# Kernel tuning notes

Hardware: AMD Instinct MI355X
Metric: run time of the kernel (lower is better)

The kernel has to match this reference:

```python
import jax, jax.numpy as jnp
import numpy as np

N = 100_000       # nodes
E = 1_600_000     # edges (avg degree 16)
D = 64            # in_dim
H = 64            # hidden width (hidden_channels = [64,64,64,64] -> 3 GCN layers)
L = 3             # num GCNConv layers
END = 128         # end_channels
EPS = 1e-5        # batchnorm eps


def setup_inputs() -> dict:
    key = jax.random.key(0)
    ks = jax.random.split(key, 8)

    def lin(k, fi, fo):
        return (jax.random.normal(k, (fi, fo), jnp.float32) / np.sqrt(fi)).astype(jnp.float32)

    X = jax.random.normal(ks[0], (N, D), jnp.float32)
    edge_index = jax.random.randint(ks[1], (2, E), 0, N)
    W_in = lin(ks[2], D, H)
    b_in = jnp.zeros((H,), jnp.float32)
    Ws = (jax.random.normal(ks[3], (L, H, H), jnp.float32) / np.sqrt(H)).astype(jnp.float32)
    bs = jnp.zeros((L, H), jnp.float32)
    gammas = jnp.ones((L, H), jnp.float32)
    betas = jnp.zeros((L, H), jnp.float32)
    W1 = lin(ks[4], H, END)
    b1 = jnp.zeros((END,), jnp.float32)
    W2 = lin(ks[5], END, 1)
    b2 = jnp.zeros((1,), jnp.float32)
    return dict(X=X, edge_index=edge_index, W_in=W_in, b_in=b_in, Ws=Ws, bs=bs,
                gammas=gammas, betas=betas, W1=W1, b1=b1, W2=W2, b2=b2)


def reference(X, edge_index, W_in, b_in, Ws, bs, gammas, betas, W1, b1, W2, b2):
    src, dst = edge_index[0], edge_index[1]
    # symmetric GCN normalization with self-loops: deg includes the self-loop (+1)
    deg = jax.ops.segment_sum(jnp.ones((E,), X.dtype), dst, num_segments=N) + 1.0
    dinv = jax.lax.rsqrt(deg)                      # deg^{-1/2}
    norm = dinv[src] * dinv[dst]                   # [E]
    self_norm = (dinv * dinv)[:, None]             # deg^{-1} for self-loop edges, [N,1]

    x = X @ W_in + b_in                            # input Linear
    for i in range(L):
        h = x @ Ws[i]                              # [N, H]
        # gather -> weight -> scatter-add (neighbor aggregation) + self-loop term + bias
        agg = jax.ops.segment_sum(h[src] * norm[:, None], dst, num_segments=N)
        h = agg + h * self_norm + bs[i]
        # BatchNorm over nodes (training-mode batch statistics)
        mean = jnp.mean(h, axis=0)
        var = jnp.var(h, axis=0)
        h = gammas[i] * (h - mean) * jax.lax.rsqrt(var + EPS) + betas[i]
        if i < L - 1:
            h = jax.nn.relu(h)
        x = h
    # OutputLayer: Linear -> act -> Linear(n_steps=1), binary=False -> no sigmoid
    h = jax.nn.relu(x @ W1 + b1)
    return h @ W2 + b2
```

## Files before the change

kernel.cpp:

```cpp
#include <hip/hip_runtime.h>

#define NN 100000
#define NE 1600000
#define NB_SCAN 391

typedef __attribute__((ext_vector_type(8))) short bf16x8;
typedef __attribute__((ext_vector_type(4))) float f32x4;

__device__ inline float b2f(unsigned short u) {
  return __uint_as_float(((unsigned)u) << 16);
}
__device__ inline unsigned short f2b(float f) {
  unsigned x = __float_as_uint(f);
  unsigned r = (x + 0x7fffu + ((x >> 16) & 1u)) >> 16;
  return (unsigned short)r;
}


__global__ void count_rank_kernel(const int* __restrict__ dst, int* __restrict__ counts,
                                  int* __restrict__ rank) {
  int i = blockIdx.x * blockDim.x + threadIdx.x;
  int st = gridDim.x * blockDim.x;
  for (; i < NE; i += st) rank[i] = atomicAdd(&counts[dst[i]], 1);
}

__global__ void scan1_kernel(const int* __restrict__ counts, int* __restrict__ offsets,
                             int* __restrict__ blocksum, float* __restrict__ dinv) {
  __shared__ int s[256];
  int t = threadIdx.x;
  int i = blockIdx.x * 256 + t;
  int v = (i < NN) ? counts[i] : 0;
  s[t] = v; __syncthreads();
  for (int off = 1; off < 256; off <<= 1) {
    int x = 0;
    if (t >= off) x = s[t - off];
    __syncthreads();
    if (t >= off) s[t] += x;
    __syncthreads();
  }
  if (i < NN) {
    offsets[i] = s[t] - v;
    dinv[i] = rsqrtf((float)v + 1.0f);
  }
  if (t == 255) blocksum[blockIdx.x] = s[255];
}

__global__ void scan2_kernel(const int* __restrict__ blocksum, int* __restrict__ blockpfx,
                             int* __restrict__ offsets) {
  __shared__ int s[512];
  int t = threadIdx.x;
  int v = (t < NB_SCAN) ? blocksum[t] : 0;
  s[t] = v; __syncthreads();
  for (int off = 1; off < 512; off <<= 1) {
    int x = 0;
    if (t >= off) x = s[t - off];
    __syncthreads();
    if (t >= off) s[t] += x;
    __syncthreads();
  }
  if (t < NB_SCAN) blockpfx[t] = s[t] - v;
  if (t == 511) offsets[NN] = s[511];
}

__global__ void scan3_kernel(int* __restrict__ offsets, const int* __restrict__ blockpfx) {
  int i = blockIdx.x * 256 + threadIdx.x;
  if (i < NN) offsets[i] += blockpfx[i >> 8];
}

__global__ void scatter_kernel(const int* __restrict__ src, const int* __restrict__ dst,
                               const int* __restrict__ offsets, const int* __restrict__ rank,
                               int* __restrict__ src_s) {
  int i = blockIdx.x * blockDim.x + threadIdx.x;
  int st = gridDim.x * blockDim.x;
  for (; i < NE; i += st) {
    int d = dst[i];
    src_s[offsets[d] + rank[i]] = src[i];
  }
}

__global__ void foldw_kernel(const float* __restrict__ W_in, const float* __restrict__ b_in,
                             const float* __restrict__ W0,
                             float* __restrict__ Wc, float* __restrict__ bc) {
  int t = threadIdx.x;
  for (int e = t; e < 4096; e += 256) {
    int i = e >> 6, j = e & 63;
    float s = 0.f;
#pragma unroll
    for (int k = 0; k < 64; ++k) s += W_in[i * 64 + k] * W0[k * 64 + j];
    Wc[e] = s;
  }
  if (t < 64) {
    float s = 0.f;
#pragma unroll
    for (int k = 0; k < 64; ++k) s += b_in[k] * W0[k * 64 + t];
    bc[t] = s;
  }
}

__global__ __launch_bounds__(256) void cvtx_kernel(const float4* __restrict__ X4,
                                                   ushort4* __restrict__ X16) {
  int i = blockIdx.x * blockDim.x + threadIdx.x;
  int st = gridDim.x * blockDim.x;
  for (; i < NN * 16; i += st) {
    float4 v = X4[i];
    ushort4 o;
    o.x = f2b(v.x); o.y = f2b(v.y); o.z = f2b(v.z); o.w = f2b(v.w);
    X16[i] = o;
  }
}


__global__ __launch_bounds__(256) void gemm_mfma_kernel(
    const unsigned short* __restrict__ x16,
    const float* __restrict__ W, const float* __restrict__ bias,
    const float* __restrict__ bnac, const float* __restrict__ dinv,
    unsigned short* __restrict__ out16) {
  __shared__ float sW[4096];
  int t = threadIdx.x;
  int lane = t & 63;
  int wv = t >> 6;
#pragma unroll
  for (int j = 0; j < 16; ++j) sW[t + 256 * j] = W[t + 256 * j];
  __syncthreads();
  int r16 = lane & 15;
  int g4 = lane >> 4;

  bf16x8 bf[4][2];
#pragma unroll
  for (int ct = 0; ct < 4; ++ct) {
#pragma unroll
    for (int kh = 0; kh < 2; ++kh) {
#pragma unroll
      for (int j = 0; j < 8; ++j) {
        int k = kh * 32 + g4 * 8 + j;
        bf[ct][kh][j] = (short)f2b(sW[k * 64 + ct * 16 + r16]);
      }
    }
  }
  float an[16], cn[16];
  if (bnac) {
#pragma unroll
    for (int kh = 0; kh < 2; ++kh) {
#pragma unroll
      for (int j = 0; j < 8; ++j) {
        int k = kh * 32 + g4 * 8 + j;
        an[kh * 8 + j] = bnac[k];
        cn[kh * 8 + j] = bnac[64 + k];
      }
    }
  }
  float bv[4];
#pragma unroll
  for (int ct = 0; ct < 4; ++ct) bv[ct] = bias ? bias[ct * 16 + r16] : 0.f;

  const int NT = NN / 16;
  int nw = gridDim.x * 4;
  for (int tile = blockIdx.x * 4 + wv; tile < NT; tile += nw) {
    int row0 = tile * 16;
    const unsigned short* xr = x16 + (size_t)(row0 + r16) * 64 + g4 * 8;
    bf16x8 alo = *(const bf16x8*)xr;
    bf16x8 ahi = *(const bf16x8*)(xr + 32);
    if (bnac) {
#pragma unroll
      for (int j = 0; j < 8; ++j) {
        float v = fmaxf(fmaf(b2f((unsigned short)alo[j]), an[j], cn[j]), 0.f);
        alo[j] = (short)f2b(v);
        float w = fmaxf(fmaf(b2f((unsigned short)ahi[j]), an[8 + j], cn[8 + j]), 0.f);
        ahi[j] = (short)f2b(w);
      }
    }
    float dv[4];
#pragma unroll
    for (int r = 0; r < 4; ++r) dv[r] = dinv[row0 + g4 * 4 + r];
#pragma unroll
    for (int ct = 0; ct < 4; ++ct) {
      f32x4 acc = {0.f, 0.f, 0.f, 0.f};
      acc = __builtin_amdgcn_mfma_f32_16x16x32_bf16(alo, bf[ct][0], acc, 0, 0, 0);
      acc = __builtin_amdgcn_mfma_f32_16x16x32_bf16(ahi, bf[ct][1], acc, 0, 0, 0);
#pragma unroll
      for (int r = 0; r < 4; ++r) {
        int grow = row0 + g4 * 4 + r;
        out16[(size_t)grow * 64 + ct * 16 + r16] = f2b((acc[r] + bv[ct]) * dv[r]);
      }
    }
  }
}


__device__ __forceinline__ void agg_slow(const unsigned short* __restrict__ xp16,
                                         const int* __restrict__ src_s,
                                         int beg, int end, int lane,
                                         float& a0, float& a1, float& a2, float& a3) {
  int deg = end - beg, done = 0;
  while (done < deg) {
    int chunk = deg - done;
    if (chunk > 64) chunk = 64;
    int idx = (lane < chunk) ? src_s[beg + done + lane] : 0;
    int j = 0;
    for (; j + 4 <= chunk; j += 4) {
      int t0 = __shfl(idx, j + 0), t1 = __shfl(idx, j + 1);
      int t2 = __shfl(idx, j + 2), t3 = __shfl(idx, j + 3);
      a0 += b2f(xp16[(size_t)t0 * 64 + lane]);
      a1 += b2f(xp16[(size_t)t1 * 64 + lane]);
      a2 += b2f(xp16[(size_t)t2 * 64 + lane]);
      a3 += b2f(xp16[(size_t)t3 * 64 + lane]);
    }
    for (; j < chunk; ++j) {
      int s = __shfl(idx, j);
      a0 += b2f(xp16[(size_t)s * 64 + lane]);
    }
    done += chunk;
  }
}

__global__ __launch_bounds__(256) void agg_kernel(
    const unsigned short* __restrict__ xp16, const int* __restrict__ offsets,
    const int* __restrict__ src_s, const float* __restrict__ dinv,
    const float* __restrict__ bvec, unsigned short* __restrict__ h2,
    float* __restrict__ bnacc) {
  int t = threadIdx.x;
  int lane = t & 63;
  int wv = t >> 6;
  float bias = bvec[lane];
  float s1 = 0.f, s2 = 0.f;
  int gw = blockIdx.x * 4 + wv;
  int nw = gridDim.x * 4;
  const int NP = NN / 2;
  for (int p = gw; p < NP; p += nw) {
    int nA = 2 * p, nB = 2 * p + 1;
    int begA = offsets[nA];
    int begB = offsets[nA + 1];
    int endB = offsets[nA + 2];
    int degA = begB - begA, degB = endB - begB;
    float a0 = b2f(xp16[(size_t)nA * 64 + lane]), a1 = 0.f, a2 = 0.f, a3 = 0.f;
    float c0 = b2f(xp16[(size_t)nB * 64 + lane]), c1 = 0.f, c2 = 0.f, c3 = 0.f;
    if (degA <= 64 && degB <= 64) {
      int idxA = (lane < degA) ? src_s[begA + lane] : 0;
      int idxB = (lane < degB) ? src_s[begB + lane] : 0;
      int ja = 0, jb = 0;
      while (ja + 8 <= degA && jb + 8 <= degB) {
        int A0 = __shfl(idxA, ja + 0), A1 = __shfl(idxA, ja + 1);
        int A2 = __shfl(idxA, ja + 2), A3 = __shfl(idxA, ja + 3);
        int A4 = __shfl(idxA, ja + 4), A5 = __shfl(idxA, ja + 5);
        int A6 = __shfl(idxA, ja + 6), A7 = __shfl(idxA, ja + 7);
        int B0 = __shfl(idxB, jb + 0), B1 = __shfl(idxB, jb + 1);
        int B2 = __shfl(idxB, jb + 2), B3 = __shfl(idxB, jb + 3);
        int B4 = __shfl(idxB, jb + 4), B5 = __shfl(idxB, jb + 5);
        int B6 = __shfl(idxB, jb + 6), B7 = __shfl(idxB, jb + 7);
        unsigned short uA0 = xp16[(size_t)A0 * 64 + lane];
        unsigned short uA1 = xp16[(size_t)A1 * 64 + lane];
        unsigned short uA2 = xp16[(size_t)A2 * 64 + lane];
        unsigned short uA3 = xp16[(size_t)A3 * 64 + lane];
        unsigned short uA4 = xp16[(size_t)A4 * 64 + lane];
        unsigned short uA5 = xp16[(size_t)A5 * 64 + lane];
        unsigned short uA6 = xp16[(size_t)A6 * 64 + lane];
        unsigned short uA7 = xp16[(size_t)A7 * 64 + lane];
        unsigned short uB0 = xp16[(size_t)B0 * 64 + lane];
        unsigned short uB1 = xp16[(size_t)B1 * 64 + lane];
        unsigned short uB2 = xp16[(size_t)B2 * 64 + lane];
        unsigned short uB3 = xp16[(size_t)B3 * 64 + lane];
        unsigned short uB4 = xp16[(size_t)B4 * 64 + lane];
        unsigned short uB5 = xp16[(size_t)B5 * 64 + lane];
        unsigned short uB6 = xp16[(size_t)B6 * 64 + lane];
        unsigned short uB7 = xp16[(size_t)B7 * 64 + lane];
        a0 += b2f(uA0) + b2f(uA4);  a1 += b2f(uA1) + b2f(uA5);
        a2 += b2f(uA2) + b2f(uA6);  a3 += b2f(uA3) + b2f(uA7);
        c0 += b2f(uB0) + b2f(uB4);  c1 += b2f(uB1) + b2f(uB5);
        c2 += b2f(uB2) + b2f(uB6);  c3 += b2f(uB3) + b2f(uB7);
        ja += 8; jb += 8;
      }
      for (; ja + 8 <= degA; ja += 8) {
        int A0 = __shfl(idxA, ja + 0), A1 = __shfl(idxA, ja + 1);
        int A2 = __shfl(idxA, ja + 2), A3 = __shfl(idxA, ja + 3);
        int A4 = __shfl(idxA, ja + 4), A5 = __shfl(idxA, ja + 5);
        int A6 = __shfl(idxA, ja + 6), A7 = __shfl(idxA, ja + 7);
        unsigned short u0 = xp16[(size_t)A0 * 64 + lane];
        unsigned short u1 = xp16[(size_t)A1 * 64 + lane];
        unsigned short u2 = xp16[(size_t)A2 * 64 + lane];
        unsigned short u3 = xp16[(size_t)A3 * 64 + lane];
        unsigned short u4 = xp16[(size_t)A4 * 64 + lane];
        unsigned short u5 = xp16[(size_t)A5 * 64 + lane];
        unsigned short u6 = xp16[(size_t)A6 * 64 + lane];
        unsigned short u7 = xp16[(size_t)A7 * 64 + lane];
        a0 += b2f(u0) + b2f(u4);  a1 += b2f(u1) + b2f(u5);
        a2 += b2f(u2) + b2f(u6);  a3 += b2f(u3) + b2f(u7);
      }
      for (; ja + 4 <= degA; ja += 4) {
        int A0 = __shfl(idxA, ja + 0), A1 = __shfl(idxA, ja + 1);
        int A2 = __shfl(idxA, ja + 2), A3 = __shfl(idxA, ja + 3);
        a0 += b2f(xp16[(size_t)A0 * 64 + lane]);
        a1 += b2f(xp16[(size_t)A1 * 64 + lane]);
        a2 += b2f(xp16[(size_t)A2 * 64 + lane]);
        a3 += b2f(xp16[(size_t)A3 * 64 + lane]);
      }
      for (; ja < degA; ++ja) {
        int s = __shfl(idxA, ja);
        a0 += b2f(xp16[(size_t)s * 64 + lane]);
      }
      for (; jb + 8 <= degB; jb += 8) {
        int B0 = __shfl(idxB, jb + 0), B1 = __shfl(idxB, jb + 1);
        int B2 = __shfl(idxB, jb + 2), B3 = __shfl(idxB, jb + 3);
        int B4 = __shfl(idxB, jb + 4), B5 = __shfl(idxB, jb + 5);
        int B6 = __shfl(idxB, jb + 6), B7 = __shfl(idxB, jb + 7);
        unsigned short u0 = xp16[(size_t)B0 * 64 + lane];
        unsigned short u1 = xp16[(size_t)B1 * 64 + lane];
        unsigned short u2 = xp16[(size_t)B2 * 64 + lane];
        unsigned short u3 = xp16[(size_t)B3 * 64 + lane];
        unsigned short u4 = xp16[(size_t)B4 * 64 + lane];
        unsigned short u5 = xp16[(size_t)B5 * 64 + lane];
        unsigned short u6 = xp16[(size_t)B6 * 64 + lane];
        unsigned short u7 = xp16[(size_t)B7 * 64 + lane];
        c0 += b2f(u0) + b2f(u4);  c1 += b2f(u1) + b2f(u5);
        c2 += b2f(u2) + b2f(u6);  c3 += b2f(u3) + b2f(u7);
      }
      for (; jb + 4 <= degB; jb += 4) {
        int B0 = __shfl(idxB, jb + 0), B1 = __shfl(idxB, jb + 1);
        int B2 = __shfl(idxB, jb + 2), B3 = __shfl(idxB, jb + 3);
        c0 += b2f(xp16[(size_t)B0 * 64 + lane]);
        c1 += b2f(xp16[(size_t)B1 * 64 + lane]);
        c2 += b2f(xp16[(size_t)B2 * 64 + lane]);
        c3 += b2f(xp16[(size_t)B3 * 64 + lane]);
      }
      for (; jb < degB; ++jb) {
        int s = __shfl(idxB, jb);
        c0 += b2f(xp16[(size_t)s * 64 + lane]);
      }
    } else {
      agg_slow(xp16, src_s, begA, begB, lane, a0, a1, a2, a3);
      agg_slow(xp16, src_s, begB, endB, lane, c0, c1, c2, c3);
    }
    float vA = ((a0 + a1) + (a2 + a3)) * dinv[nA] + bias;
    float vB = ((c0 + c1) + (c2 + c3)) * dinv[nB] + bias;
    h2[(size_t)nA * 64 + lane] = f2b(vA);
    h2[(size_t)nB * 64 + lane] = f2b(vB);
    s1 += vA + vB;
    s2 += vA * vA + vB * vB;
  }
  __shared__ float ls[4][2][64];
  ls[wv][0][lane] = s1;
  ls[wv][1][lane] = s2;
  __syncthreads();
  if (wv == 0) {
    float a = ls[0][0][lane] + ls[1][0][lane] + ls[2][0][lane] + ls[3][0][lane];
    float b = ls[0][1][lane] + ls[1][1][lane] + ls[2][1][lane] + ls[3][1][lane];
    atomicAdd(&bnacc[lane], a);
    atomicAdd(&bnacc[64 + lane], b);
  }
}

__global__ void bn_finalize_kernel(const float* __restrict__ bnacc,
                                   const float* __restrict__ gamma,
                                   const float* __restrict__ beta,
                                   float* __restrict__ bnac) {
  int ch = threadIdx.x;
  float mean = bnacc[ch] * (1.0f / NN);
  float var = bnacc[64 + ch] * (1.0f / NN) - mean * mean;
  float istd = rsqrtf(var + 1e-5f);
  float a = gamma[ch] * istd;
  bnac[ch] = a;
  bnac[64 + ch] = beta[ch] - mean * a;
}


__global__ __launch_bounds__(256) void out_kernel(
    const unsigned short* __restrict__ x, const float* __restrict__ bnac,
    const float* __restrict__ W1, const float* __restrict__ b1,
    const float* __restrict__ W2, const float* __restrict__ b2,
    float* __restrict__ out) {
  __shared__ float sW1[64][128];
  __shared__ float sx[16][64];
  __shared__ float sz[16][128];
  __shared__ float sW2[128];
  int t = threadIdx.x;
  int row0 = blockIdx.x * 16;
#pragma unroll
  for (int j = 0; j < 32; ++j) {
    int e = t + 256 * j;
    sW1[e >> 7][e & 127] = W1[e];
  }
  if (t < 128) sW2[t] = W2[t];
  {
    int c64 = t & 63;
    float a = bnac[c64], c = bnac[64 + c64];
#pragma unroll
    for (int j = 0; j < 4; ++j) {
      int e = t + 256 * j;
      int r = e >> 6;
      int grow = row0 + r;
      float v = (grow < NN) ? b2f(x[(size_t)grow * 64 + c64]) : 0.f;
      sx[r][c64] = fmaf(v, a, c);
    }
  }
  __syncthreads();

  int col = t & 127;
  int rg = t >> 7;
  float b1v = b1[col];
  float acc[8];
#pragma unroll
  for (int r = 0; r < 8; ++r) acc[r] = 0.f;
#pragma unroll 4
  for (int k = 0; k < 64; k += 4) {
    float w0 = sW1[k + 0][col], w1 = sW1[k + 1][col];
    float w2 = sW1[k + 2][col], w3 = sW1[k + 3][col];
#pragma unroll
    for (int r = 0; r < 8; ++r) {
      float4 xv = *(const float4*)&sx[rg * 8 + r][k];
      acc[r] = fmaf(xv.w, w3, fmaf(xv.z, w2, fmaf(xv.y, w1, fmaf(xv.x, w0, acc[r]))));
    }
  }
#pragma unroll
  for (int r = 0; r < 8; ++r) sz[rg * 8 + r][col] = fmaxf(acc[r] + b1v, 0.f);
  __syncthreads();

  {
    int row = t >> 4, g = t & 15;
    const float4* zr = (const float4*)&sz[row][0];
    const float4* wp = (const float4*)sW2;
    float4 z0 = zr[g * 2], z1 = zr[g * 2 + 1];
    float4 w0 = wp[g * 2], w1 = wp[g * 2 + 1];
    float p = z0.x * w0.x + z0.y * w0.y + z0.z * w0.z + z0.w * w0.w
            + z1.x * w1.x + z1.y * w1.y + z1.z * w1.z + z1.w * w1.w;
    p += __shfl_down(p, 8);
    p += __shfl_down(p, 4);
    p += __shfl_down(p, 2);
    p += __shfl_down(p, 1);
    int grow = row0 + row;
    if (g == 0 && grow < NN) out[grow] = p + b2[0];
  }
}


extern "C" void kernel_launch(void* const* d_in, const int* in_sizes, int n_in,
                              void* d_out, int out_size, void* d_ws, size_t ws_size,
                              hipStream_t stream) {
  const float* X = (const float*)d_in[0];
  const int* edge = (const int*)d_in[1];
  const int* esrc = edge;
  const int* edst = edge + NE;
  const float* W_in = (const float*)d_in[2];
  const float* b_in = (const float*)d_in[3];
  const float* Ws = (const float*)d_in[4];
  const float* bs = (const float*)d_in[5];
  const float* gammas = (const float*)d_in[6];
  const float* betas = (const float*)d_in[7];
  const float* W1 = (const float*)d_in[8];
  const float* b1 = (const float*)d_in[9];
  const float* W2 = (const float*)d_in[10];
  const float* b2 = (const float*)d_in[11];
  float* out = (float*)d_out;

  char* base = (char*)d_ws;
  size_t o = 0;
  auto alloc = [&](size_t bytes) {
    o = (o + 255) & ~(size_t)255;
    void* p = base + o;
    o += bytes;
    return p;
  };
  int* counts = (int*)alloc((size_t)NN * 4);
  int* offsets = (int*)alloc((size_t)(NN + 1) * 4);
  int* blocksum = (int*)alloc(512 * 4);
  int* blockpfx = (int*)alloc(512 * 4);
  int* rank = (int*)alloc((size_t)NE * 4);
  int* src_s = (int*)alloc((size_t)NE * 4);
  float* dinv = (float*)alloc((size_t)NN * 4);
  unsigned short* X16 = (unsigned short*)alloc((size_t)NN * 64 * 2);
  unsigned short* bufA = (unsigned short*)alloc((size_t)NN * 64 * 2);
  unsigned short* bufB = (unsigned short*)alloc((size_t)NN * 64 * 2);
  unsigned short* hbuf16 = (unsigned short*)alloc((size_t)NN * 64 * 2);
  float* bnacc = (float*)alloc(3 * 128 * 4);
  float* bnpar = (float*)alloc(3 * 128 * 4);
  float* Wc = (float*)alloc(4096 * 4);
  float* bc = (float*)alloc(64 * 4);

  hipMemsetAsync(counts, 0, (size_t)NN * 4, stream);
  hipMemsetAsync(bnacc, 0, 3 * 128 * 4, stream);

  foldw_kernel<<<1, 256, 0, stream>>>(W_in, b_in, Ws, Wc, bc);
  cvtx_kernel<<<2048, 256, 0, stream>>>((const float4*)X, (ushort4*)X16);
  count_rank_kernel<<<2048, 256, 0, stream>>>(edst, counts, rank);
  scan1_kernel<<<NB_SCAN, 256, 0, stream>>>(counts, offsets, blocksum, dinv);
  scan2_kernel<<<1, 512, 0, stream>>>(blocksum, blockpfx, offsets);
  scan3_kernel<<<NB_SCAN, 256, 0, stream>>>(offsets, blockpfx);
  scatter_kernel<<<2048, 256, 0, stream>>>(esrc, edst, offsets, rank, src_s);

  const int GEMM_GRID = (NN + 15) / 16;
  unsigned short* xbufs[2] = {bufA, bufB};
  const unsigned short* xcur = nullptr;
  for (int i = 0; i < 3; ++i) {
    if (i == 0) {
      gemm_mfma_kernel<<<1563, 256, 0, stream>>>(X16, Wc, bc, nullptr, dinv, hbuf16);
    } else {
      gemm_mfma_kernel<<<1563, 256, 0, stream>>>(xcur, Ws + (size_t)i * 64 * 64, nullptr,
                                                 bnpar + (size_t)(i - 1) * 128,
                                                 dinv, hbuf16);
    }
    unsigned short* xnext = xbufs[i & 1];
    agg_kernel<<<2048, 256, 0, stream>>>(hbuf16, offsets, src_s, dinv,
                                         bs + (size_t)i * 64, xnext,
                                         bnacc + (size_t)i * 128);
    bn_finalize_kernel<<<1, 64, 0, stream>>>(bnacc + (size_t)i * 128,
                                             gammas + (size_t)i * 64,
                                             betas + (size_t)i * 64,
                                             bnpar + (size_t)i * 128);
    xcur = xnext;
  }
  out_kernel<<<GEMM_GRID, 256, 0, stream>>>(xcur, bnpar + 2 * 128, W1, b1, W2, b2, out);
}
```

Measured before the change: 589.7 us.

## Fuse input conversion and BN finalize into GEMMs, MFMA output head, 16-bit ranks

Removes the separate fp32-to-bf16 conversion of X by letting the first GEMM read fp32 directly. Drops the bn_finalize kernels by computing mean, variance and scale per thread inside the consumer kernels. Rewrites the output head to use bf16 MFMA with the second linear layer fused as a shuffle reduction. Stores edge ranks as 16-bit. Together these cut kernel launches and memory traffic, at the cost of redundant per-thread BN math and rank values that overflow if any node has more than 65535 in-edges.

```diff
diff --git a/kernel.cpp b/kernel.cpp
--- a/kernel.cpp
+++ b/kernel.cpp
@@ -18,10 +18,10 @@
 
 
 __global__ void count_rank_kernel(const int* __restrict__ dst, int* __restrict__ counts,
-                                  int* __restrict__ rank) {
+                                  unsigned short* __restrict__ rank) {
   int i = blockIdx.x * blockDim.x + threadIdx.x;
   int st = gridDim.x * blockDim.x;
-  for (; i < NE; i += st) rank[i] = atomicAdd(&counts[dst[i]], 1);
+  for (; i < NE; i += st) rank[i] = (unsigned short)atomicAdd(&counts[dst[i]], 1);
 }
 
 __global__ void scan1_kernel(const int* __restrict__ counts, int* __restrict__ offsets,
@@ -68,13 +68,14 @@
 }
 
 __global__ void scatter_kernel(const int* __restrict__ src, const int* __restrict__ dst,
-                               const int* __restrict__ offsets, const int* __restrict__ rank,
+                               const int* __restrict__ offsets,
+                               const unsigned short* __restrict__ rank,
                                int* __restrict__ src_s) {
   int i = blockIdx.x * blockDim.x + threadIdx.x;
   int st = gridDim.x * blockDim.x;
   for (; i < NE; i += st) {
     int d = dst[i];
-    src_s[offsets[d] + rank[i]] = src[i];
+    src_s[offsets[d] + (int)rank[i]] = src[i];
   }
 }
 
@@ -97,23 +98,12 @@
   }
 }
 
-__global__ __launch_bounds__(256) void cvtx_kernel(const float4* __restrict__ X4,
-                                                   ushort4* __restrict__ X16) {
-  int i = blockIdx.x * blockDim.x + threadIdx.x;
-  int st = gridDim.x * blockDim.x;
-  for (; i < NN * 16; i += st) {
-    float4 v = X4[i];
-    ushort4 o;
-    o.x = f2b(v.x); o.y = f2b(v.y); o.z = f2b(v.z); o.w = f2b(v.w);
-    X16[i] = o;
-  }
-}
-
 
 __global__ __launch_bounds__(256) void gemm_mfma_kernel(
-    const unsigned short* __restrict__ x16,
+    const void* __restrict__ xin, int xbf16,
     const float* __restrict__ W, const float* __restrict__ bias,
-    const float* __restrict__ bnac, const float* __restrict__ dinv,
+    const float* __restrict__ bnacc, const float* __restrict__ gamma,
+    const float* __restrict__ beta, const float* __restrict__ dinv,
     unsigned short* __restrict__ out16) {
   __shared__ float sW[4096];
   int t = threadIdx.x;
@@ -138,14 +128,17 @@
     }
   }
   float an[16], cn[16];
-  if (bnac) {
+  if (bnacc) {
 #pragma unroll
     for (int kh = 0; kh < 2; ++kh) {
 #pragma unroll
       for (int j = 0; j < 8; ++j) {
         int k = kh * 32 + g4 * 8 + j;
-        an[kh * 8 + j] = bnac[k];
-        cn[kh * 8 + j] = bnac[64 + k];
+        float mean = bnacc[k] * (1.0f / NN);
+        float var = bnacc[64 + k] * (1.0f / NN) - mean * mean;
+        float a = gamma[k] * rsqrtf(var + 1e-5f);
+        an[kh * 8 + j] = a;
+        cn[kh * 8 + j] = beta[k] - mean * a;
       }
     }
   }
@@ -157,10 +150,27 @@
   int nw = gridDim.x * 4;
   for (int tile = blockIdx.x * 4 + wv; tile < NT; tile += nw) {
     int row0 = tile * 16;
-    const unsigned short* xr = x16 + (size_t)(row0 + r16) * 64 + g4 * 8;
-    bf16x8 alo = *(const bf16x8*)xr;
-    bf16x8 ahi = *(const bf16x8*)(xr + 32);
-    if (bnac) {
+    bf16x8 alo, ahi;
+    if (xbf16) {
+      const unsigned short* xr = (const unsigned short*)xin + (size_t)(row0 + r16) * 64 + g4 * 8;
+      alo = *(const bf16x8*)xr;
+      ahi = *(const bf16x8*)(xr + 32);
+    } else {
+      const float* xr = (const float*)xin + (size_t)(row0 + r16) * 64 + g4 * 8;
+      float4 f0 = *(const float4*)xr;
+      float4 f1 = *(const float4*)(xr + 4);
+      float4 f2_ = *(const float4*)(xr + 32);
+      float4 f3_ = *(const float4*)(xr + 36);
+      alo[0] = (short)f2b(f0.x); alo[1] = (short)f2b(f0.y);
+      alo[2] = (short)f2b(f0.z); alo[3] = (short)f2b(f0.w);
+      alo[4] = (short)f2b(f1.x); alo[5] = (short)f2b(f1.y);
+      alo[6] = (short)f2b(f1.z); alo[7] = (short)f2b(f1.w);
+      ahi[0] = (short)f2b(f2_.x); ahi[1] = (short)f2b(f2_.y);
+      ahi[2] = (short)f2b(f2_.z); ahi[3] = (short)f2b(f2_.w);
+      ahi[4] = (short)f2b(f3_.x); ahi[5] = (short)f2b(f3_.y);
+      ahi[6] = (short)f2b(f3_.z); ahi[7] = (short)f2b(f3_.w);
+    }
+    if (bnacc) {
 #pragma unroll
       for (int j = 0; j < 8; ++j) {
         float v = fmaxf(fmaf(b2f((unsigned short)alo[j]), an[j], cn[j]), 0.f);
@@ -348,85 +358,94 @@
   }
 }
 
-__global__ void bn_finalize_kernel(const float* __restrict__ bnacc,
-                                   const float* __restrict__ gamma,
-                                   const float* __restrict__ beta,
-                                   float* __restrict__ bnac) {
-  int ch = threadIdx.x;
-  float mean = bnacc[ch] * (1.0f / NN);
-  float var = bnacc[64 + ch] * (1.0f / NN) - mean * mean;
-  float istd = rsqrtf(var + 1e-5f);
-  float a = gamma[ch] * istd;
-  bnac[ch] = a;
-  bnac[64 + ch] = beta[ch] - mean * a;
-}
-
-
-__global__ __launch_bounds__(256) void out_kernel(
-    const unsigned short* __restrict__ x, const float* __restrict__ bnac,
+
+__global__ __launch_bounds__(256) void out_mfma_kernel(
+    const unsigned short* __restrict__ x16,
+    const float* __restrict__ bnacc, const float* __restrict__ gamma,
+    const float* __restrict__ beta,
     const float* __restrict__ W1, const float* __restrict__ b1,
     const float* __restrict__ W2, const float* __restrict__ b2,
     float* __restrict__ out) {
-  __shared__ float sW1[64][128];
-  __shared__ float sx[16][64];
-  __shared__ float sz[16][128];
-  __shared__ float sW2[128];
+  __shared__ float sW1[8192];
   int t = threadIdx.x;
-  int row0 = blockIdx.x * 16;
-#pragma unroll
-  for (int j = 0; j < 32; ++j) {
-    int e = t + 256 * j;
-    sW1[e >> 7][e & 127] = W1[e];
-  }
-  if (t < 128) sW2[t] = W2[t];
-  {
-    int c64 = t & 63;
-    float a = bnac[c64], c = bnac[64 + c64];
-#pragma unroll
-    for (int j = 0; j < 4; ++j) {
-      int e = t + 256 * j;
-      int r = e >> 6;
-      int grow = row0 + r;
-      float v = (grow < NN) ? b2f(x[(size_t)grow * 64 + c64]) : 0.f;
-      sx[r][c64] = fmaf(v, a, c);
-    }
-  }
+  int lane = t & 63;
+  int wv = t >> 6;
+#pragma unroll
+  for (int j = 0; j < 32; ++j) sW1[t + 256 * j] = W1[t + 256 * j];
   __syncthreads();
-
-  int col = t & 127;
-  int rg = t >> 7;
-  float b1v = b1[col];
-  float acc[8];
-#pragma unroll
-  for (int r = 0; r < 8; ++r) acc[r] = 0.f;
-#pragma unroll 4
-  for (int k = 0; k < 64; k += 4) {
-    float w0 = sW1[k + 0][col], w1 = sW1[k + 1][col];
-    float w2 = sW1[k + 2][col], w3 = sW1[k + 3][col];
-#pragma unroll
-    for (int r = 0; r < 8; ++r) {
-      float4 xv = *(const float4*)&sx[rg * 8 + r][k];
-      acc[r] = fmaf(xv.w, w3, fmaf(xv.z, w2, fmaf(xv.y, w1, fmaf(xv.x, w0, acc[r]))));
-    }
-  }
-#pragma unroll
-  for (int r = 0; r < 8; ++r) sz[rg * 8 + r][col] = fmaxf(acc[r] + b1v, 0.f);
-  __syncthreads();
-
-  {
-    int row = t >> 4, g = t & 15;
-    const float4* zr = (const float4*)&sz[row][0];
-    const float4* wp = (const float4*)sW2;
-    float4 z0 = zr[g * 2], z1 = zr[g * 2 + 1];
-    float4 w0 = wp[g * 2], w1 = wp[g * 2 + 1];
-    float p = z0.x * w0.x + z0.y * w0.y + z0.z * w0.z + z0.w * w0.w
-            + z1.x * w1.x + z1.y * w1.y + z1.z * w1.z + z1.w * w1.w;
-    p += __shfl_down(p, 8);
-    p += __shfl_down(p, 4);
-    p += __shfl_down(p, 2);
-    p += __shfl_down(p, 1);
-    int grow = row0 + row;
-    if (g == 0 && grow < NN) out[grow] = p + b2[0];
+  int r16 = lane & 15;
+  int g4 = lane >> 4;
+
+  bf16x8 bw[8][2];
+#pragma unroll
+  for (int ct = 0; ct < 8; ++ct) {
+#pragma unroll
+    for (int kh = 0; kh < 2; ++kh) {
+#pragma unroll
+      for (int j = 0; j < 8; ++j) {
+        int k = kh * 32 + g4 * 8 + j;
+        bw[ct][kh][j] = (short)f2b(sW1[k * 128 + ct * 16 + r16]);
+      }
+    }
+  }
+  float an[16], cn[16];
+#pragma unroll
+  for (int kh = 0; kh < 2; ++kh) {
+#pragma unroll
+    for (int j = 0; j < 8; ++j) {
+      int k = kh * 32 + g4 * 8 + j;
+      float mean = bnacc[k] * (1.0f / NN);
+      float var = bnacc[64 + k] * (1.0f / NN) - mean * mean;
+      float a = gamma[k] * rsqrtf(var + 1e-5f);
+      an[kh * 8 + j] = a;
+      cn[kh * 8 + j] = beta[k] - mean * a;
+    }
+  }
+  float b1v[8], w2v[8];
+#pragma unroll
+  for (int ct = 0; ct < 8; ++ct) {
+    b1v[ct] = b1[ct * 16 + r16];
+    w2v[ct] = W2[ct * 16 + r16];
+  }
+  float bias2 = b2[0];
+
+  const int NT = NN / 16;
+  int nw = gridDim.x * 4;
+  for (int tile = blockIdx.x * 4 + wv; tile < NT; tile += nw) {
+    int row0 = tile * 16;
+    const unsigned short* xr = x16 + (size_t)(row0 + r16) * 64 + g4 * 8;
+    bf16x8 alo = *(const bf16x8*)xr;
+    bf16x8 ahi = *(const bf16x8*)(xr + 32);
+#pragma unroll
+    for (int j = 0; j < 8; ++j) {
+      alo[j] = (short)f2b(fmaf(b2f((unsigned short)alo[j]), an[j], cn[j]));
+      ahi[j] = (short)f2b(fmaf(b2f((unsigned short)ahi[j]), an[8 + j], cn[8 + j]));
+    }
+    float p0 = 0.f, p1 = 0.f, p2 = 0.f, p3 = 0.f;
+#pragma unroll
+    for (int ct = 0; ct < 8; ++ct) {
+      f32x4 acc = {0.f, 0.f, 0.f, 0.f};
+      acc = __builtin_amdgcn_mfma_f32_16x16x32_bf16(alo, bw[ct][0], acc, 0, 0, 0);
+      acc = __builtin_amdgcn_mfma_f32_16x16x32_bf16(ahi, bw[ct][1], acc, 0, 0, 0);
+      p0 += fmaxf(acc[0] + b1v[ct], 0.f) * w2v[ct];
+      p1 += fmaxf(acc[1] + b1v[ct], 0.f) * w2v[ct];
+      p2 += fmaxf(acc[2] + b1v[ct], 0.f) * w2v[ct];
+      p3 += fmaxf(acc[3] + b1v[ct], 0.f) * w2v[ct];
+    }
+#pragma unroll
+    for (int m = 1; m < 16; m <<= 1) {
+      p0 += __shfl_xor(p0, m);
+      p1 += __shfl_xor(p1, m);
+      p2 += __shfl_xor(p2, m);
+      p3 += __shfl_xor(p3, m);
+    }
+    if (r16 == 0) {
+      int rbase = row0 + g4 * 4;
+      out[rbase + 0] = p0 + bias2;
+      out[rbase + 1] = p1 + bias2;
+      out[rbase + 2] = p2 + bias2;
+      out[rbase + 3] = p3 + bias2;
+    }
   }
 }
 
@@ -462,15 +481,13 @@
   int* offsets = (int*)alloc((size_t)(NN + 1) * 4);
   int* blocksum = (int*)alloc(512 * 4);
   int* blockpfx = (int*)alloc(512 * 4);
-  int* rank = (int*)alloc((size_t)NE * 4);
+  unsigned short* rank = (unsigned short*)alloc((size_t)NE * 2);
   int* src_s = (int*)alloc((size_t)NE * 4);
   float* dinv = (float*)alloc((size_t)NN * 4);
-  unsigned short* X16 = (unsigned short*)alloc((size_t)NN * 64 * 2);
   unsigned short* bufA = (unsigned short*)alloc((size_t)NN * 64 * 2);
   unsigned short* bufB = (unsigned short*)alloc((size_t)NN * 64 * 2);
   unsigned short* hbuf16 = (unsigned short*)alloc((size_t)NN * 64 * 2);
   float* bnacc = (float*)alloc(3 * 128 * 4);
-  float* bnpar = (float*)alloc(3 * 128 * 4);
   float* Wc = (float*)alloc(4096 * 4);
   float* bc = (float*)alloc(64 * 4);
 
@@ -478,33 +495,31 @@
   hipMemsetAsync(bnacc, 0, 3 * 128 * 4, stream);
 
   foldw_kernel<<<1, 256, 0, stream>>>(W_in, b_in, Ws, Wc, bc);
-  cvtx_kernel<<<2048, 256, 0, stream>>>((const float4*)X, (ushort4*)X16);
   count_rank_kernel<<<2048, 256, 0, stream>>>(edst, counts, rank);
   scan1_kernel<<<NB_SCAN, 256, 0, stream>>>(counts, offsets, blocksum, dinv);
   scan2_kernel<<<1, 512, 0, stream>>>(blocksum, blockpfx, offsets);
   scan3_kernel<<<NB_SCAN, 256, 0, stream>>>(offsets, blockpfx);
   scatter_kernel<<<2048, 256, 0, stream>>>(esrc, edst, offsets, rank, src_s);
 
-  const int GEMM_GRID = (NN + 15) / 16;
   unsigned short* xbufs[2] = {bufA, bufB};
   const unsigned short* xcur = nullptr;
   for (int i = 0; i < 3; ++i) {
     if (i == 0) {
-      gemm_mfma_kernel<<<1563, 256, 0, stream>>>(X16, Wc, bc, nullptr, dinv, hbuf16);
+      gemm_mfma_kernel<<<1563, 256, 0, stream>>>(X, 0, Wc, bc, nullptr, nullptr, nullptr,
+                                                 dinv, hbuf16);
     } else {
-      gemm_mfma_kernel<<<1563, 256, 0, stream>>>(xcur, Ws + (size_t)i * 64 * 64, nullptr,
-                                                 bnpar + (size_t)(i - 1) * 128,
+      gemm_mfma_kernel<<<1563, 256, 0, stream>>>(xcur, 1, Ws + (size_t)i * 64 * 64, nullptr,
+                                                 bnacc + (size_t)(i - 1) * 128,
+                                                 gammas + (size_t)(i - 1) * 64,
+                                                 betas + (size_t)(i - 1) * 64,
                                                  dinv, hbuf16);
     }
     unsigned short* xnext = xbufs[i & 1];
     agg_kernel<<<2048, 256, 0, stream>>>(hbuf16, offsets, src_s, dinv,
                                          bs + (size_t)i * 64, xnext,
                                          bnacc + (size_t)i * 128);
-    bn_finalize_kernel<<<1, 64, 0, stream>>>(bnacc + (size_t)i * 128,
-                                             gammas + (size_t)i * 64,
-                                             betas + (size_t)i * 64,
-                                             bnpar + (size_t)i * 128);
     xcur = xnext;
   }
-  out_kernel<<<GEMM_GRID, 256, 0, stream>>>(xcur, bnpar + 2 * 128, W1, b1, W2, b2, out);
-}
+  out_mfma_kernel<<<1563, 256, 0, stream>>>(xcur, bnacc + 2 * 128, gammas + 2 * 64,
+                                            betas + 2 * 64, W1, b1, W2, b2, out);
+}
```

Result: faster. 549.9 us (-6.8%).
